# Performance work log

Measured on AMD Instinct MI355X. Metric: run time of the kernel, lower is better.

Reference implementation:

```python
import jax, jax.numpy as jnp
import numpy as np
from jax import lax

B, L, C = 4, 4096, 512
H = 8           # head_num
D = C // H      # head dim = 64
RR = 4          # reduction_ratio -> reducer conv kernel 7, stride 4
KS = 3          # MixFFN depthwise kernel
ER = 4          # expansion ratio -> 2048 channels
EPS = 1e-5      # torch LayerNorm default eps


def _ln(x, g, b):
    # LayerNorm over last axis, affine per-channel
    m = jnp.mean(x, axis=-1, keepdims=True)
    v = jnp.mean(jnp.square(x - m), axis=-1, keepdims=True)
    return (x - m) * lax.rsqrt(v + EPS) * g + b


def setup_inputs() -> dict:
    key = jax.random.key(0)
    ks = jax.random.split(key, 9)
    s = lambda fan: 1.0 / np.sqrt(fan)
    return {
        "x": jax.random.normal(ks[0], (B, L, C), jnp.float32),
        "w_q": jax.random.normal(ks[1], (C, C), jnp.float32) * s(C),
        "w_k": jax.random.normal(ks[2], (C, C), jnp.float32) * s(C),
        "w_v": jax.random.normal(ks[3], (C, C), jnp.float32) * s(C),
        "w_o": jax.random.normal(ks[4], (C, C), jnp.float32) * s(C),
        "w_red": jax.random.normal(ks[5], (C, C, 2 * RR - 1), jnp.float32) * s(C * (2 * RR - 1)),
        "w_ffn1": jax.random.normal(ks[6], (C, C), jnp.float32) * s(C),
        "w_ffn_dw": jax.random.normal(ks[7], (C * ER, 1, KS), jnp.float32) * s(KS),
        "w_ffn2": jax.random.normal(ks[8], (C, C * ER), jnp.float32) * s(C * ER),
        "ln_gamma": jnp.ones((6, C), jnp.float32),
        "ln_beta": jnp.zeros((6, C), jnp.float32),
    }


def reference(x, w_q, w_k, w_v, w_o, w_red, w_ffn1, w_ffn_dw, w_ffn2, ln_gamma, ln_beta):
    # ln indices: 0=ln1(pre-attn), 1=ln(reducer), 2=ln_q, 3=ln_k, 4=ln_v, 5=ln2(pre-ffn)
    residual = x
    h = _ln(x, ln_gamma[0], ln_beta[0])  # B L C

    # --- spatial-reduction for K/V: reflect-pad strided conv + LN ---
    p = (2 * RR - 1) // 2
    hr = jnp.transpose(h, (0, 2, 1))  # B C L
    hr = jnp.pad(hr, ((0, 0), (0, 0), (p, p)), mode="reflect")
    red = lax.conv_general_dilated(hr, w_red, window_strides=(RR,), padding="VALID",
                                   dimension_numbers=("NCH", "OIH", "NCH"))  # B C Lr
    red = jnp.transpose(red, (0, 2, 1))  # B Lr C
    red = _ln(red, ln_gamma[1], ln_beta[1])

    # --- QKV projections + LayerNorms ---
    q = _ln(h @ w_q.T, ln_gamma[2], ln_beta[2])      # B L C
    k = _ln(red @ w_k.T, ln_gamma[3], ln_beta[3])    # B Lr C
    v = _ln(red @ w_v.T, ln_gamma[4], ln_beta[4])    # B Lr C

    Lr = k.shape[1]
    q = q.reshape(B, L, H, D).transpose(0, 2, 1, 3)   # B h L d
    k = k.reshape(B, Lr, H, D).transpose(0, 2, 1, 3)  # B h Lr d
    v = v.reshape(B, Lr, H, D).transpose(0, 2, 1, 3)

    scores = jnp.einsum("bhqd,bhkd->bhqk", q, k) / jnp.sqrt(jnp.float32(D))
    attn = jax.nn.softmax(scores, axis=-1)
    out = jnp.einsum("bhqk,bhkd->bhqd", attn, v)
    out = out.transpose(0, 2, 1, 3).reshape(B, L, C)
    out = out @ w_o.T

    h2 = out + residual
    residual2 = h2
    f = _ln(h2, ln_gamma[5], ln_beta[5])  # B L C

    # --- MixFFN: 1x1 conv -> depthwise reflect conv (groups=C, out=ER*C) -> GELU -> 1x1 conv ---
    f = jnp.transpose(f, (0, 2, 1))  # B C L
    f = jnp.einsum("oi,bil->bol", w_ffn1, f)  # 1x1, C->C
    pk = (KS - 1) // 2
    fp = jnp.pad(f, ((0, 0), (0, 0), (pk, pk)), mode="reflect")
    f = lax.conv_general_dilated(fp, w_ffn_dw, window_strides=(1,), padding="VALID",
                                 dimension_numbers=("NCH", "OIH", "NCH"),
                                 feature_group_count=C)  # B (ER*C) L
    f = jax.nn.gelu(f, approximate=False)  # torch nn.GELU() is exact erf
    f = jnp.einsum("oi,bil->bol", w_ffn2, f)  # 1x1, ER*C->C
    f = jnp.transpose(f, (0, 2, 1))  # B L C

    return f + residual2
```

## Files before the change

### kernel.cpp

```cpp
#include <hip/hip_runtime.h>
#include <math.h>

typedef __attribute__((ext_vector_type(8))) short short8;
typedef __attribute__((ext_vector_type(4))) float f32x4;
typedef unsigned short u16;
typedef unsigned int u32;
typedef unsigned long long u64;

namespace {
constexpr int kB = 4;
constexpr int kL = 4096;
constexpr int kC = 512;
constexpr int kH = 8;
constexpr int kLr = 1024;
constexpr int kCH = 2048;
constexpr int kKred = 3584;
constexpr float kEps = 1e-5f;
}

__device__ __forceinline__ float bf2f(u16 u) { return __uint_as_float(((u32)u) << 16); }
__device__ __forceinline__ u16 f2bf(float f) {
  u32 u = __float_as_uint(f);
  u32 r = (u + 0x7fffu + ((u >> 16) & 1u)) >> 16;
  return (u16)r;
}
__device__ __forceinline__ u32 cvtpk(float lo, float hi) {
  u32 r;
  asm("v_cvt_pk_bf16_f32 %0, %1, %2" : "=v"(r) : "v"(lo), "v"(hi));
  return r;
}

__device__ __forceinline__ void gload_lds16(const void* g, void* l) {
  __builtin_amdgcn_global_load_lds(
      (const __attribute__((address_space(1))) unsigned int*)g,
      (__attribute__((address_space(3))) unsigned int*)l, 16, 0, 0);
}

__device__ __forceinline__ short8 ldsfrag(const u16* base, int row, int col16) {
  return *(const short8*)(base + (size_t)(((row << 3) + (col16 ^ (row & 7))) << 3));
}

__global__ __launch_bounds__(256) void cvt_weights_kernel(
    const float* __restrict__ w_q, const float* __restrict__ w_k,
    const float* __restrict__ w_v, const float* __restrict__ w_o,
    const float* __restrict__ w_f1, const float* __restrict__ w_f2,
    u16* __restrict__ dst) {
  const int i = (blockIdx.x * 256 + threadIdx.x) * 4;
  const int seg = i >> 18;
  const float* src;
  int off;
  if (seg < 5) {
    src = (seg == 0) ? w_q : (seg == 1) ? w_k : (seg == 2) ? w_v : (seg == 3) ? w_o : w_f1;
    off = i & 262143;
  } else {
    src = w_f2;
    off = i - 1310720;
  }
  const float4 v = *(const float4*)(src + off);
  u16 o[4] = {f2bf(v.x), f2bf(v.y), f2bf(v.z), f2bf(v.w)};
  *(u64*)(dst + i) = *(u64*)o;
}

__global__ __launch_bounds__(256) void repack_wred_kernel(const float* __restrict__ src,
                                                          u16* __restrict__ dst) {
  const int idx = blockIdx.x * 256 + threadIdx.x;
  if (idx >= kC * kKred) return;
  const int o = idx / kKred;
  const int rem = idx - o * kKred;
  const int t = rem >> 9;
  const int i = rem & (kC - 1);
  dst[idx] = f2bf(src[(size_t)(o * kC + i) * 7 + t]);
}

__global__ __launch_bounds__(256) void ln_bf16_kernel(const float* __restrict__ in,
                                                      u16* __restrict__ out,
                                                      const float* __restrict__ g,
                                                      const float* __restrict__ be) {
  const int row = blockIdx.x;
  const int tid = threadIdx.x;
  const float2 v = *(const float2*)(in + (size_t)row * kC + tid * 2);
  float s = v.x + v.y;
  float ss = v.x * v.x + v.y * v.y;
#pragma unroll
  for (int off = 32; off > 0; off >>= 1) {
    s += __shfl_down(s, off);
    ss += __shfl_down(ss, off);
  }
  __shared__ float wsum[4][2];
  __shared__ float mi[2];
  const int wave = tid >> 6, lane = tid & 63;
  if (lane == 0) { wsum[wave][0] = s; wsum[wave][1] = ss; }
  __syncthreads();
  if (tid == 0) {
    const float S = wsum[0][0] + wsum[1][0] + wsum[2][0] + wsum[3][0];
    const float SS = wsum[0][1] + wsum[1][1] + wsum[2][1] + wsum[3][1];
    const float mean = S * (1.0f / kC);
    const float var = SS * (1.0f / kC) - mean * mean;
    mi[0] = mean;
    mi[1] = rsqrtf(var + kEps);
  }
  __syncthreads();
  const float mean = mi[0], inv = mi[1];
  const float2 gg = *(const float2*)(g + tid * 2);
  const float2 bb = *(const float2*)(be + tid * 2);
  u16 o2[2] = {f2bf((v.x - mean) * inv * gg.x + bb.x), f2bf((v.y - mean) * inv * gg.y + bb.y)};
  *(u32*)(out + (size_t)row * kC + tid * 2) = *(u32*)o2;
}

__global__ __launch_bounds__(256) void reduce2_ln_kernel(const float* __restrict__ P,
                                                         u16* __restrict__ out,
                                                         const float* __restrict__ g,
                                                         const float* __restrict__ be) {
  const int row = blockIdx.x;
  const int tid = threadIdx.x;
  const size_t stride = (size_t)kB * kLr * kC;
  float2 v = make_float2(0.f, 0.f);
#pragma unroll
  for (int z = 0; z < 2; ++z) {
    const float2 p = *(const float2*)(P + z * stride + (size_t)row * kC + tid * 2);
    v.x += p.x;
    v.y += p.y;
  }
  float s = v.x + v.y;
  float ss = v.x * v.x + v.y * v.y;
#pragma unroll
  for (int off = 32; off > 0; off >>= 1) {
    s += __shfl_down(s, off);
    ss += __shfl_down(ss, off);
  }
  __shared__ float wsum[4][2];
  __shared__ float mi[2];
  const int wave = tid >> 6, lane = tid & 63;
  if (lane == 0) { wsum[wave][0] = s; wsum[wave][1] = ss; }
  __syncthreads();
  if (tid == 0) {
    const float S = wsum[0][0] + wsum[1][0] + wsum[2][0] + wsum[3][0];
    const float SS = wsum[0][1] + wsum[1][1] + wsum[2][1] + wsum[3][1];
    const float mean = S * (1.0f / kC);
    const float var = SS * (1.0f / kC) - mean * mean;
    mi[0] = mean;
    mi[1] = rsqrtf(var + kEps);
  }
  __syncthreads();
  const float mean = mi[0], inv = mi[1];
  const float2 gg = *(const float2*)(g + tid * 2);
  const float2 bb = *(const float2*)(be + tid * 2);
  u16 o2[2] = {f2bf((v.x - mean) * inv * gg.x + bb.x), f2bf((v.y - mean) * inv * gg.y + bb.y)};
  *(u32*)(out + (size_t)row * kC + tid * 2) = *(u32*)o2;
}

__global__ __launch_bounds__(256) void dwgelu_kernel(const u16* __restrict__ f1,
                                                     const float* __restrict__ wdw,
                                                     u16* __restrict__ fdw) {
  const int row = blockIdx.x;
  const int l = row & (kL - 1);
  const int rb = row - l;
  const int cc0 = threadIdx.x * 8;
  const int cg = cc0 >> 2;
  const int lm = (l == 0) ? 1 : l - 1;
  const int lp = (l == kL - 1) ? kL - 2 : l + 1;
  const u32 xm = *(const u32*)(f1 + (size_t)(rb + lm) * kC + cg);
  const u32 x0 = *(const u32*)(f1 + (size_t)(rb + l) * kC + cg);
  const u32 xp = *(const u32*)(f1 + (size_t)(rb + lp) * kC + cg);
  const float xml = bf2f((u16)xm), xmh = bf2f((u16)(xm >> 16));
  const float x0l = bf2f((u16)x0), x0h = bf2f((u16)(x0 >> 16));
  const float xpl = bf2f((u16)xp), xph = bf2f((u16)(xp >> 16));
  float wv[24];
#pragma unroll
  for (int t = 0; t < 6; ++t)
    *(float4*)&wv[t * 4] = *(const float4*)(wdw + (size_t)cc0 * 3 + t * 4);
  short8 pk;
#pragma unroll
  for (int j = 0; j < 8; ++j) {
    const float a_ = (j < 4) ? xml : xmh;
    const float b_ = (j < 4) ? x0l : x0h;
    const float c_ = (j < 4) ? xpl : xph;
    const float dw = wv[j * 3] * a_ + wv[j * 3 + 1] * b_ + wv[j * 3 + 2] * c_;
    pk[j] = (short)f2bf(0.5f * dw * (1.0f + erff(dw * 0.70710678118654752440f)));
  }
  *(short8*)(fdw + (size_t)row * kCH + cc0) = pk;
}

__global__ __launch_bounds__(256) void mgemm_red_kernel(
    const u16* __restrict__ A, const u16* __restrict__ W, float* __restrict__ OutF,
    int M, int N, int K) {
  __shared__ __align__(16) u16 As[128 * 64];
  __shared__ __align__(16) u16 Bs[128 * 64];
  const int tid = threadIdx.x;
  const int lane = tid & 63, w = tid >> 6;
  const int m0 = blockIdx.y * 128, n0 = blockIdx.x * 128;
  const int wm = (w >> 1) * 64, wn = (w & 1) * 64;
  const f32x4 zero = {0.f, 0.f, 0.f, 0.f};
  f32x4 acc[4][4];
#pragma unroll
  for (int i = 0; i < 4; ++i)
#pragma unroll
    for (int j = 0; j < 4; ++j) acc[i][j] = zero;

  const int kc = K / gridDim.z;
  const int kBeg = blockIdx.z * kc, kEnd = kBeg + kc;
  float* outp = OutF + (size_t)blockIdx.z * M * N;

  for (int k0 = kBeg; k0 < kEnd; k0 += 64) {
    __syncthreads();
#pragma unroll
    for (int c = 0; c < 4; ++c) {
      const int ci = w * 4 + c;
      const int idx = ci * 64 + lane;
      const int row = idx >> 3, s = idx & 7;
      const int c16 = s ^ (row & 7);
      gload_lds16(W + (size_t)(n0 + row) * K + k0 + c16 * 8, (char*)Bs + ci * 1024);
    }
#pragma unroll
    for (int c = 0; c < 4; ++c) {
      const int ci = w * 4 + c;
      const int idx = ci * 64 + lane;
      const int row = idx >> 3, s = idx & 7;
      const int c16 = s ^ (row & 7);
      const int m = m0 + row;
      const int b = m >> 10, lr = m & (kLr - 1);
      const int k = k0 + c16 * 8;
      const int t = k >> 9, i = k & (kC - 1);
      int pos = 4 * lr + t - 3;
      pos = pos < 0 ? -pos : (pos >= kL ? 2 * kL - 2 - pos : pos);
      gload_lds16(A + ((size_t)(b << 12) + pos) * kC + i, (char*)As + ci * 1024);
    }
    __syncthreads();
#pragma unroll
    for (int kst = 0; kst < 2; ++kst) {
      short8 af[4], bfr[4];
      const int c16 = kst * 4 + (lane >> 4);
#pragma unroll
      for (int mb = 0; mb < 4; ++mb) af[mb] = ldsfrag(As, wm + mb * 16 + (lane & 15), c16);
#pragma unroll
      for (int nb = 0; nb < 4; ++nb) bfr[nb] = ldsfrag(Bs, wn + nb * 16 + (lane & 15), c16);
#pragma unroll
      for (int mb = 0; mb < 4; ++mb)
#pragma unroll
        for (int nb = 0; nb < 4; ++nb)
          acc[mb][nb] = __builtin_amdgcn_mfma_f32_16x16x32_bf16(af[mb], bfr[nb], acc[mb][nb], 0, 0, 0);
    }
  }
#pragma unroll
  for (int mb = 0; mb < 4; ++mb)
#pragma unroll
    for (int r = 0; r < 4; ++r) {
      const int row = m0 + wm + mb * 16 + ((lane >> 4) << 2) + r;
#pragma unroll
      for (int nb = 0; nb < 4; ++nb)
        outp[(size_t)row * N + n0 + wn + nb * 16 + (lane & 15)] = acc[mb][nb][r];
    }
}

__global__ __launch_bounds__(256) void mgemm_res_kernel(
    const u16* __restrict__ A, const u16* __restrict__ W,
    const float* __restrict__ Res, float* __restrict__ OutF, int M, int N, int K) {
  __shared__ __align__(16) u16 As[128 * 64];
  __shared__ __align__(16) u16 Bs[128 * 64];
  const int tid = threadIdx.x;
  const int lane = tid & 63, w = tid >> 6;
  const int m0 = blockIdx.y * 128, n0 = blockIdx.x * 128;
  const int wm = (w >> 1) * 64, wn = (w & 1) * 64;
  const f32x4 zero = {0.f, 0.f, 0.f, 0.f};
  f32x4 acc[4][4];
#pragma unroll
  for (int i = 0; i < 4; ++i)
#pragma unroll
    for (int j = 0; j < 4; ++j) acc[i][j] = zero;

  for (int k0 = 0; k0 < K; k0 += 64) {
    __syncthreads();
#pragma unroll
    for (int c = 0; c < 4; ++c) {
      const int ci = w * 4 + c;
      const int idx = ci * 64 + lane;
      const int row = idx >> 3, s = idx & 7;
      const int c16 = s ^ (row & 7);
      gload_lds16(W + (size_t)(n0 + row) * K + k0 + c16 * 8, (char*)Bs + ci * 1024);
    }
#pragma unroll
    for (int c = 0; c < 4; ++c) {
      const int ci = w * 4 + c;
      const int idx = ci * 64 + lane;
      const int row = idx >> 3, s = idx & 7;
      const int c16 = s ^ (row & 7);
      gload_lds16(A + (size_t)(m0 + row) * K + k0 + c16 * 8, (char*)As + ci * 1024);
    }
    __syncthreads();
#pragma unroll
    for (int kst = 0; kst < 2; ++kst) {
      short8 af[4], bfr[4];
      const int c16 = kst * 4 + (lane >> 4);
#pragma unroll
      for (int mb = 0; mb < 4; ++mb) af[mb] = ldsfrag(As, wm + mb * 16 + (lane & 15), c16);
#pragma unroll
      for (int nb = 0; nb < 4; ++nb) bfr[nb] = ldsfrag(Bs, wn + nb * 16 + (lane & 15), c16);
#pragma unroll
      for (int mb = 0; mb < 4; ++mb)
#pragma unroll
        for (int nb = 0; nb < 4; ++nb)
          acc[mb][nb] = __builtin_amdgcn_mfma_f32_16x16x32_bf16(af[mb], bfr[nb], acc[mb][nb], 0, 0, 0);
    }
  }
#pragma unroll
  for (int mb = 0; mb < 4; ++mb)
#pragma unroll
    for (int r = 0; r < 4; ++r) {
      const int row = m0 + wm + mb * 16 + ((lane >> 4) << 2) + r;
#pragma unroll
      for (int nb = 0; nb < 4; ++nb) {
        const size_t off = (size_t)row * N + n0 + wn + nb * 16 + (lane & 15);
        OutF[off] = acc[mb][nb][r] + Res[off];
      }
    }
}

template <int EPI>
__global__ __launch_bounds__(512) void gemm512_kernel(
    const u16* __restrict__ A, const u16* __restrict__ W,
    const float* __restrict__ Res, float* __restrict__ OutF,
    u16* __restrict__ OutB, u16* __restrict__ OutB2,
    int K, const float* __restrict__ gam, const float* __restrict__ bet, float oscale) {
  constexpr bool RES_ = (EPI == 3);
  constexpr bool LN_ = (EPI == 1 || EPI == 2 || EPI == 3);
  __shared__ __align__(16) u16 As[64 * 64];
  __shared__ __align__(16) u16 Bs[512 * 64];
  const int tid = threadIdx.x;
  const int lane = tid & 63, w = tid >> 6;
  const int l15 = lane & 15, g = lane >> 4;
  const int m0 = blockIdx.y * 64;
  const int n0 = blockIdx.x * 512;
  const int wn = w << 6;
  const f32x4 zero = {0.f, 0.f, 0.f, 0.f};
  f32x4 acc[4][4];
#pragma unroll
  for (int i = 0; i < 4; ++i)
#pragma unroll
    for (int j = 0; j < 4; ++j) acc[i][j] = zero;

  for (int k0 = 0; k0 < K; k0 += 64) {
    __syncthreads();
#pragma unroll
    for (int c = 0; c < 8; ++c) {
      const int cg = (w << 3) + c;
      const int idx = (cg << 6) + lane;
      const int row = idx >> 3, sl = idx & 7;
      const int c16 = sl ^ (row & 7);
      gload_lds16(W + (size_t)(n0 + row) * K + k0 + (c16 << 3), (char*)Bs + cg * 1024);
    }
    {
      const int idx = (w << 6) + lane;
      const int row = idx >> 3, sl = idx & 7;
      const int c16 = sl ^ (row & 7);
      gload_lds16(A + (size_t)(m0 + row) * K + k0 + (c16 << 3), (char*)As + w * 1024);
    }
    __syncthreads();
#pragma unroll
    for (int kst = 0; kst < 2; ++kst) {
      const int c16 = (kst << 2) + g;
      short8 af[4], bfr[4];
#pragma unroll
      for (int mb = 0; mb < 4; ++mb) af[mb] = ldsfrag(As, (mb << 4) + l15, c16);
#pragma unroll
      for (int nb = 0; nb < 4; ++nb) bfr[nb] = ldsfrag(Bs, wn + (nb << 4) + l15, c16);
#pragma unroll
      for (int mb = 0; mb < 4; ++mb)
#pragma unroll
        for (int nb = 0; nb < 4; ++nb)
          acc[mb][nb] = __builtin_amdgcn_mfma_f32_16x16x32_bf16(af[mb], bfr[nb], acc[mb][nb], 0, 0, 0);
    }
  }

  if (RES_) {
#pragma unroll
    for (int mb = 0; mb < 4; ++mb)
#pragma unroll
      for (int r = 0; r < 4; ++r) {
        const int grow = m0 + (mb << 4) + (g << 2) + r;
#pragma unroll
        for (int nb = 0; nb < 4; ++nb)
          acc[mb][nb][r] += Res[(size_t)grow * kC + wn + (nb << 4) + l15];
      }
  }
  float* rs = (float*)As;
  float* rs2 = rs + 512;
  float2* minv = (float2*)(rs2 + 512);
  if (LN_) {
    __syncthreads();
#pragma unroll
    for (int mb = 0; mb < 4; ++mb)
#pragma unroll
      for (int r = 0; r < 4; ++r) {
        float s = acc[mb][0][r] + acc[mb][1][r] + acc[mb][2][r] + acc[mb][3][r];
        float s2 = acc[mb][0][r] * acc[mb][0][r] + acc[mb][1][r] * acc[mb][1][r] +
                   acc[mb][2][r] * acc[mb][2][r] + acc[mb][3][r] * acc[mb][3][r];
        s += __shfl_xor(s, 1); s += __shfl_xor(s, 2); s += __shfl_xor(s, 4); s += __shfl_xor(s, 8);
        s2 += __shfl_xor(s2, 1); s2 += __shfl_xor(s2, 2); s2 += __shfl_xor(s2, 4); s2 += __shfl_xor(s2, 8);
        if (l15 == 0) {
          const int row = (mb << 4) + (g << 2) + r;
          rs[(w << 6) + row] = s;
          rs2[(w << 6) + row] = s2;
        }
      }
    __syncthreads();
    if (tid < 64) {
      float S = 0.f, SS = 0.f;
#pragma unroll
      for (int w8 = 0; w8 < 8; ++w8) { S += rs[(w8 << 6) + tid]; SS += rs2[(w8 << 6) + tid]; }
      const float mean = S * (1.0f / 512.0f);
      const float var = SS * (1.0f / 512.0f) - mean * mean;
      minv[tid] = make_float2(mean, rsqrtf(var + kEps));
    }
    __syncthreads();
  }
  float g4[4], b4[4];
  if (LN_) {
    const float* gp = (EPI == 2 && blockIdx.x) ? gam + kC : gam;
    const float* bp = (EPI == 2 && blockIdx.x) ? bet + kC : bet;
#pragma unroll
    for (int nb = 0; nb < 4; ++nb) {
      const int cc = wn + (nb << 4) + l15;
      g4[nb] = gp[cc];
      b4[nb] = bp[cc];
    }
  }
#pragma unroll
  for (int mb = 0; mb < 4; ++mb) {
#pragma unroll
    for (int r = 0; r < 4; ++r) {
      const int row = (mb << 4) + (g << 2) + r;
      const int grow = m0 + row;
      float2 mi = make_float2(0.f, 0.f);
      if (LN_) mi = minv[row];
#pragma unroll
      for (int nb = 0; nb < 4; ++nb) {
        const int cc = wn + (nb << 4) + l15;
        const float vv = acc[mb][nb][r];
        if (EPI == 0) {
          OutB[(size_t)grow * kC + cc] = f2bf(vv);
        } else if (EPI == 1) {
          OutB[(size_t)grow * kC + cc] = f2bf(((vv - mi.x) * mi.y * g4[nb] + b4[nb]) * oscale);
        } else if (EPI == 2) {
          const float lv = (vv - mi.x) * mi.y * g4[nb] + b4[nb];
          if (blockIdx.x == 0) {
            OutB[(size_t)grow * kC + cc] = f2bf(lv);
          } else {
            const int b = grow >> 10, lr = grow & (kLr - 1);
            const int hh = cc >> 6, d = cc & 63;
            OutB2[((size_t)((b << 3) + hh) * 64 + d) * kLr + lr] = f2bf(lv);
          }
        } else {
          OutF[(size_t)grow * kC + cc] = vv;
          OutB[(size_t)grow * kC + cc] = f2bf((vv - mi.x) * mi.y * g4[nb] + b4[nb]);
        }
      }
    }
  }
}

__global__ __launch_bounds__(256) void attn_mfma_kernel(
    const u16* __restrict__ q, const u16* __restrict__ k,
    const u16* __restrict__ vt, u16* __restrict__ o) {
  __shared__ __align__(16) u16 Qs[128 * 64];
  __shared__ __align__(16) u16 Ks[2][64 * 64];
  __shared__ __align__(16) u16 Vs[2][64 * 64];
  __shared__ __align__(16) u16 Ps[4][32 * 64];
  const int tid = threadIdx.x;
  const int lane = tid & 63, w = tid >> 6;
  const int qt = blockIdx.x, h = blockIdx.y, b = blockIdx.z;
  const int q0 = qt << 7;
  const int l15 = lane & 15, g = lane >> 4;

#pragma unroll
  for (int c = 0; c < 4; ++c) {
    const int ci = (w << 2) + c;
    const int a16 = (ci << 6) + lane;
    const int r = a16 >> 3, sl = a16 & 7;
    gload_lds16(q + (size_t)((b << 12) + q0 + r) * kC + (h << 6) + ((sl ^ (r & 7)) << 3),
                (char*)Qs + ci * 1024);
  }
#pragma unroll
  for (int c = 0; c < 2; ++c) {
    const int ci = (w << 1) + c;
    const int a16 = (ci << 6) + lane;
    const int r = a16 >> 3, sl = a16 & 7;
    const int c16 = sl ^ (r & 7);
    gload_lds16(k + (size_t)((b << 10) + r) * kC + (h << 6) + (c16 << 3), (char*)Ks[0] + ci * 1024);
    gload_lds16(vt + (size_t)(((b << 3) + h) * 64 + r) * kLr + (c16 << 3), (char*)Vs[0] + ci * 1024);
  }

  const f32x4 zero = {0.f, 0.f, 0.f, 0.f};
  float m2[2] = {-1e30f, -1e30f};
  float l2[2] = {0.f, 0.f};
  f32x4 accO[2][4];
#pragma unroll
  for (int s_ = 0; s_ < 2; ++s_)
#pragma unroll
    for (int d = 0; d < 4; ++d) accO[s_][d] = zero;

  __syncthreads();

  for (int t = 0; t < kLr / 64; ++t) {
    const int cur = t & 1;
    if (t < kLr / 64 - 1) {
      const int kv0 = (t + 1) << 6;
#pragma unroll
      for (int c = 0; c < 2; ++c) {
        const int ci = (w << 1) + c;
        const int a16 = (ci << 6) + lane;
        const int r = a16 >> 3, sl = a16 & 7;
        const int c16 = sl ^ (r & 7);
        gload_lds16(k + (size_t)((b << 10) + kv0 + r) * kC + (h << 6) + (c16 << 3),
                    (char*)Ks[cur ^ 1] + ci * 1024);
        gload_lds16(vt + (size_t)(((b << 3) + h) * 64 + r) * kLr + kv0 + (c16 << 3),
                    (char*)Vs[cur ^ 1] + ci * 1024);
      }
    }
    f32x4 st[2][4];
#pragma unroll
    for (int s_ = 0; s_ < 2; ++s_)
#pragma unroll
      for (int nb = 0; nb < 4; ++nb) st[s_][nb] = zero;
    __builtin_amdgcn_s_setprio(1);
#pragma unroll
    for (int kst = 0; kst < 2; ++kst) {
      const int c16 = (kst << 2) + g;
      const short8 bq0 = ldsfrag(Qs, (w << 5) + l15, c16);
      const short8 bq1 = ldsfrag(Qs, (w << 5) + 16 + l15, c16);
#pragma unroll
      for (int nb = 0; nb < 4; ++nb) {
        const short8 ak = ldsfrag(Ks[cur], (nb << 4) + l15, c16);
        st[0][nb] = __builtin_amdgcn_mfma_f32_16x16x32_bf16(ak, bq0, st[0][nb], 0, 0, 0);
        st[1][nb] = __builtin_amdgcn_mfma_f32_16x16x32_bf16(ak, bq1, st[1][nb], 0, 0, 0);
      }
    }
    __builtin_amdgcn_s_setprio(0);
    bool sk[2];
#pragma unroll
    for (int s_ = 0; s_ < 2; ++s_) {
      float pm = -1e30f;
#pragma unroll
      for (int nb = 0; nb < 4; ++nb)
#pragma unroll
        for (int r = 0; r < 4; ++r) pm = fmaxf(pm, st[s_][nb][r]);
      pm = fmaxf(pm, __shfl_xor(pm, 16));
      pm = fmaxf(pm, __shfl_xor(pm, 32));
      sk[s_] = __all(pm - m2[s_] <= 8.0f);
      float scl = 1.0f;
      if (!sk[s_]) {
        const float mnew = fmaxf(m2[s_], pm);
        scl = __expf(m2[s_] - mnew);
        m2[s_] = mnew;
      }
      float ps = 0.f;
#pragma unroll
      for (int nb = 0; nb < 4; ++nb)
#pragma unroll
        for (int r = 0; r < 4; ++r) {
          const float e = __expf(st[s_][nb][r] - m2[s_]);
          st[s_][nb][r] = e;
          ps += e;
        }
      ps += __shfl_xor(ps, 16);
      ps += __shfl_xor(ps, 32);
      l2[s_] = l2[s_] * scl + ps;
      char* pw = (char*)&Ps[w][0];
      const int row = (s_ << 4) + l15;
#pragma unroll
      for (int nb = 0; nb < 4; ++nb) {
        const u32 lo = cvtpk(st[s_][nb][0], st[s_][nb][1]);
        const u32 hi = cvtpk(st[s_][nb][2], st[s_][nb][3]);
        const int slot = ((nb << 1) + (g >> 1)) ^ (row & 7);
        *(u64*)(pw + (row << 7) + (slot << 4) + ((g & 1) << 3)) = ((u64)hi << 32) | lo;
      }
      if (!sk[s_]) {
        const float scl2 = scl;
        float scA[4];
#pragma unroll
        for (int r = 0; r < 4; ++r) scA[r] = __shfl(scl2, (g << 2) + r);
#pragma unroll
        for (int d = 0; d < 4; ++d)
#pragma unroll
          for (int r = 0; r < 4; ++r) accO[s_][d][r] *= scA[r];
      }
    }
    __builtin_amdgcn_s_setprio(1);
#pragma unroll
    for (int kvs = 0; kvs < 2; ++kvs) {
      const int c16 = (kvs << 2) + g;
      const short8 ap0 = ldsfrag(&Ps[w][0], l15, c16);
      const short8 ap1 = ldsfrag(&Ps[w][0], 16 + l15, c16);
#pragma unroll
      for (int d = 0; d < 4; ++d) {
        const short8 bv = ldsfrag(Vs[cur], (d << 4) + l15, c16);
        accO[0][d] = __builtin_amdgcn_mfma_f32_16x16x32_bf16(ap0, bv, accO[0][d], 0, 0, 0);
        accO[1][d] = __builtin_amdgcn_mfma_f32_16x16x32_bf16(ap1, bv, accO[1][d], 0, 0, 0);
      }
    }
    __builtin_amdgcn_s_setprio(0);
    __syncthreads();
  }
#pragma unroll
  for (int s_ = 0; s_ < 2; ++s_) {
    float li[4];
#pragma unroll
    for (int r = 0; r < 4; ++r) li[r] = 1.0f / __shfl(l2[s_], (g << 2) + r);
    const int qg = (b << 12) + q0 + (w << 5) + (s_ << 4) + (g << 2);
#pragma unroll
    for (int d = 0; d < 4; ++d)
#pragma unroll
      for (int r = 0; r < 4; ++r)
        o[(size_t)(qg + r) * kC + (h << 6) + (d << 4) + l15] = f2bf(accO[s_][d][r] * li[r]);
  }
}

extern "C" void kernel_launch(void* const* d_in, const int* in_sizes, int n_in,
                              void* d_out, int out_size, void* d_ws, size_t ws_size,
                              hipStream_t stream) {
  const float* x      = (const float*)d_in[0];
  const float* w_q    = (const float*)d_in[1];
  const float* w_k    = (const float*)d_in[2];
  const float* w_v    = (const float*)d_in[3];
  const float* w_o    = (const float*)d_in[4];
  const float* w_red  = (const float*)d_in[5];
  const float* w_ffn1 = (const float*)d_in[6];
  const float* w_dw   = (const float*)d_in[7];
  const float* w_ffn2 = (const float*)d_in[8];
  const float* gam    = (const float*)d_in[9];
  const float* bet    = (const float*)d_in[10];
  float* out = (float*)d_out;

  const size_t nBLC = (size_t)kB * kL * kC;
  const size_t nBLrC = (size_t)kB * kLr * kC;
  u16* us = (u16*)d_ws;
  u16* wqb   = us;
  u16* wkb   = wqb + 262144;
  u16* wob   = wkb + 2 * 262144;
  u16* wf1b  = wob + 262144;
  u16* wf2b  = wf1b + 262144;
  u16* wredb = wf2b + 1048576;
  u16* h_b   = wredb + 1835008;
  u16* q_b   = h_b + nBLC;
  u16* red_b = q_b + nBLC;
  u16* k_b   = red_b + nBLrC;
  u16* vt_b  = k_b + nBLrC;
  float* S   = (float*)(vt_b + nBLrC);
  u16* fdw   = q_b;

  cvt_weights_kernel<<<2304, 256, 0, stream>>>(w_q, w_k, w_v, w_o, w_ffn1, w_ffn2, wqb);
  repack_wred_kernel<<<7168, 256, 0, stream>>>(w_red, wredb);

  ln_bf16_kernel<<<kB * kL, 256, 0, stream>>>(x, h_b, gam, bet);
  mgemm_red_kernel<<<dim3(4, 32, 2), 256, 0, stream>>>(h_b, wredb, S, kB * kLr, kC, kKred);
  reduce2_ln_kernel<<<kB * kLr, 256, 0, stream>>>(S, red_b, gam + kC, bet + kC);
  gemm512_kernel<1><<<dim3(1, 256), 512, 0, stream>>>(
      h_b, wqb, nullptr, nullptr, q_b, nullptr, kC, gam + 2 * kC, bet + 2 * kC, 0.125f);
  gemm512_kernel<2><<<dim3(2, 64), 512, 0, stream>>>(
      red_b, wkb, nullptr, nullptr, k_b, vt_b, kC, gam + 3 * kC, bet + 3 * kC, 1.0f);
  attn_mfma_kernel<<<dim3(kL / 128, kH, kB), 256, 0, stream>>>(q_b, k_b, vt_b, h_b);
  gemm512_kernel<3><<<dim3(1, 256), 512, 0, stream>>>(
      h_b, wob, x, out, q_b, nullptr, kC, gam + 5 * kC, bet + 5 * kC, 1.0f);
  gemm512_kernel<0><<<dim3(1, 256), 512, 0, stream>>>(
      q_b, wf1b, nullptr, nullptr, h_b, nullptr, kC, nullptr, nullptr, 1.0f);
  dwgelu_kernel<<<kB * kL, 256, 0, stream>>>(h_b, w_dw, fdw);
  mgemm_res_kernel<<<dim3(4, 128), 256, 0, stream>>>(fdw, wf2b, out, out, kB * kL, kC, kCH);
}
```

Before: 320.2 us.

## Double-buffer GEMM LDS tiles and halve attention query tile per block

All three GEMM kernels now keep two LDS buffers and issue the loads for the next K-tile before computing on the current one, so global-to-LDS transfers overlap MFMA work and each iteration needs one barrier instead of two. The attention kernel drops from 128 to 64 queries per block (16 per wave), which doubles the grid and lowers register and LDS use per block. The cost is double the GEMM LDS footprint (about 72KB for gemm512), which can lower occupancy, and more reloads of K/V across the extra attention blocks.

```diff
diff --git a/kernel.cpp b/kernel.cpp
--- a/kernel.cpp
+++ b/kernel.cpp
@@ -184,8 +184,8 @@
 __global__ __launch_bounds__(256) void mgemm_red_kernel(
     const u16* __restrict__ A, const u16* __restrict__ W, float* __restrict__ OutF,
     int M, int N, int K) {
-  __shared__ __align__(16) u16 As[128 * 64];
-  __shared__ __align__(16) u16 Bs[128 * 64];
+  __shared__ __align__(16) u16 As[2][128 * 64];
+  __shared__ __align__(16) u16 Bs[2][128 * 64];
   const int tid = threadIdx.x;
   const int lane = tid & 63, w = tid >> 6;
   const int m0 = blockIdx.y * 128, n0 = blockIdx.x * 128;
@@ -198,48 +198,48 @@
     for (int j = 0; j < 4; ++j) acc[i][j] = zero;
 
   const int kc = K / gridDim.z;
-  const int kBeg = blockIdx.z * kc, kEnd = kBeg + kc;
+  const int kBeg = blockIdx.z * kc;
   float* outp = OutF + (size_t)blockIdx.z * M * N;
 
-  for (int k0 = kBeg; k0 < kEnd; k0 += 64) {
-    __syncthreads();
+  auto stage = [&](int buf, int k0) {
 #pragma unroll
     for (int c = 0; c < 4; ++c) {
       const int ci = w * 4 + c;
       const int idx = ci * 64 + lane;
       const int row = idx >> 3, s = idx & 7;
       const int c16 = s ^ (row & 7);
-      gload_lds16(W + (size_t)(n0 + row) * K + k0 + c16 * 8, (char*)Bs + ci * 1024);
-    }
-#pragma unroll
-    for (int c = 0; c < 4; ++c) {
-      const int ci = w * 4 + c;
-      const int idx = ci * 64 + lane;
-      const int row = idx >> 3, s = idx & 7;
-      const int c16 = s ^ (row & 7);
+      gload_lds16(W + (size_t)(n0 + row) * K + k0 + c16 * 8, (char*)Bs[buf] + ci * 1024);
       const int m = m0 + row;
       const int b = m >> 10, lr = m & (kLr - 1);
       const int k = k0 + c16 * 8;
       const int t = k >> 9, i = k & (kC - 1);
       int pos = 4 * lr + t - 3;
       pos = pos < 0 ? -pos : (pos >= kL ? 2 * kL - 2 - pos : pos);
-      gload_lds16(A + ((size_t)(b << 12) + pos) * kC + i, (char*)As + ci * 1024);
-    }
-    __syncthreads();
+      gload_lds16(A + ((size_t)(b << 12) + pos) * kC + i, (char*)As[buf] + ci * 1024);
+    }
+  };
+
+  const int nk = kc >> 6;
+  stage(0, kBeg);
+  __syncthreads();
+  for (int t = 0; t < nk; ++t) {
+    const int cur = t & 1;
+    if (t + 1 < nk) stage(cur ^ 1, kBeg + ((t + 1) << 6));
 #pragma unroll
     for (int kst = 0; kst < 2; ++kst) {
       short8 af[4], bfr[4];
       const int c16 = kst * 4 + (lane >> 4);
 #pragma unroll
-      for (int mb = 0; mb < 4; ++mb) af[mb] = ldsfrag(As, wm + mb * 16 + (lane & 15), c16);
-#pragma unroll
-      for (int nb = 0; nb < 4; ++nb) bfr[nb] = ldsfrag(Bs, wn + nb * 16 + (lane & 15), c16);
+      for (int mb = 0; mb < 4; ++mb) af[mb] = ldsfrag(As[cur], wm + mb * 16 + (lane & 15), c16);
+#pragma unroll
+      for (int nb = 0; nb < 4; ++nb) bfr[nb] = ldsfrag(Bs[cur], wn + nb * 16 + (lane & 15), c16);
 #pragma unroll
       for (int mb = 0; mb < 4; ++mb)
 #pragma unroll
         for (int nb = 0; nb < 4; ++nb)
           acc[mb][nb] = __builtin_amdgcn_mfma_f32_16x16x32_bf16(af[mb], bfr[nb], acc[mb][nb], 0, 0, 0);
     }
+    __syncthreads();
   }
 #pragma unroll
   for (int mb = 0; mb < 4; ++mb)
@@ -255,8 +255,8 @@
 __global__ __launch_bounds__(256) void mgemm_res_kernel(
     const u16* __restrict__ A, const u16* __restrict__ W,
     const float* __restrict__ Res, float* __restrict__ OutF, int M, int N, int K) {
-  __shared__ __align__(16) u16 As[128 * 64];
-  __shared__ __align__(16) u16 Bs[128 * 64];
+  __shared__ __align__(16) u16 As[2][128 * 64];
+  __shared__ __align__(16) u16 Bs[2][128 * 64];
   const int tid = threadIdx.x;
   const int lane = tid & 63, w = tid >> 6;
   const int m0 = blockIdx.y * 128, n0 = blockIdx.x * 128;
@@ -268,39 +268,39 @@
 #pragma unroll
     for (int j = 0; j < 4; ++j) acc[i][j] = zero;
 
-  for (int k0 = 0; k0 < K; k0 += 64) {
-    __syncthreads();
+  auto stage = [&](int buf, int k0) {
 #pragma unroll
     for (int c = 0; c < 4; ++c) {
       const int ci = w * 4 + c;
       const int idx = ci * 64 + lane;
       const int row = idx >> 3, s = idx & 7;
       const int c16 = s ^ (row & 7);
-      gload_lds16(W + (size_t)(n0 + row) * K + k0 + c16 * 8, (char*)Bs + ci * 1024);
-    }
-#pragma unroll
-    for (int c = 0; c < 4; ++c) {
-      const int ci = w * 4 + c;
-      const int idx = ci * 64 + lane;
-      const int row = idx >> 3, s = idx & 7;
-      const int c16 = s ^ (row & 7);
-      gload_lds16(A + (size_t)(m0 + row) * K + k0 + c16 * 8, (char*)As + ci * 1024);
-    }
-    __syncthreads();
+      gload_lds16(W + (size_t)(n0 + row) * K + k0 + c16 * 8, (char*)Bs[buf] + ci * 1024);
+      gload_lds16(A + (size_t)(m0 + row) * K + k0 + c16 * 8, (char*)As[buf] + ci * 1024);
+    }
+  };
+
+  const int nk = K >> 6;
+  stage(0, 0);
+  __syncthreads();
+  for (int t = 0; t < nk; ++t) {
+    const int cur = t & 1;
+    if (t + 1 < nk) stage(cur ^ 1, (t + 1) << 6);
 #pragma unroll
     for (int kst = 0; kst < 2; ++kst) {
       short8 af[4], bfr[4];
       const int c16 = kst * 4 + (lane >> 4);
 #pragma unroll
-      for (int mb = 0; mb < 4; ++mb) af[mb] = ldsfrag(As, wm + mb * 16 + (lane & 15), c16);
-#pragma unroll
-      for (int nb = 0; nb < 4; ++nb) bfr[nb] = ldsfrag(Bs, wn + nb * 16 + (lane & 15), c16);
+      for (int mb = 0; mb < 4; ++mb) af[mb] = ldsfrag(As[cur], wm + mb * 16 + (lane & 15), c16);
+#pragma unroll
+      for (int nb = 0; nb < 4; ++nb) bfr[nb] = ldsfrag(Bs[cur], wn + nb * 16 + (lane & 15), c16);
 #pragma unroll
       for (int mb = 0; mb < 4; ++mb)
 #pragma unroll
         for (int nb = 0; nb < 4; ++nb)
           acc[mb][nb] = __builtin_amdgcn_mfma_f32_16x16x32_bf16(af[mb], bfr[nb], acc[mb][nb], 0, 0, 0);
     }
+    __syncthreads();
   }
 #pragma unroll
   for (int mb = 0; mb < 4; ++mb)
@@ -323,8 +323,8 @@
     int K, const float* __restrict__ gam, const float* __restrict__ bet, float oscale) {
   constexpr bool RES_ = (EPI == 3);
   constexpr bool LN_ = (EPI == 1 || EPI == 2 || EPI == 3);
-  __shared__ __align__(16) u16 As[64 * 64];
-  __shared__ __align__(16) u16 Bs[512 * 64];
+  __shared__ __align__(16) u16 As[2][64 * 64];
+  __shared__ __align__(16) u16 Bs[2][512 * 64];
   const int tid = threadIdx.x;
   const int lane = tid & 63, w = tid >> 6;
   const int l15 = lane & 15, g = lane >> 4;
@@ -338,37 +338,42 @@
 #pragma unroll
     for (int j = 0; j < 4; ++j) acc[i][j] = zero;
 
-  for (int k0 = 0; k0 < K; k0 += 64) {
-    __syncthreads();
+  auto stage = [&](int buf, int k0) {
 #pragma unroll
     for (int c = 0; c < 8; ++c) {
       const int cg = (w << 3) + c;
       const int idx = (cg << 6) + lane;
       const int row = idx >> 3, sl = idx & 7;
       const int c16 = sl ^ (row & 7);
-      gload_lds16(W + (size_t)(n0 + row) * K + k0 + (c16 << 3), (char*)Bs + cg * 1024);
-    }
-    {
-      const int idx = (w << 6) + lane;
-      const int row = idx >> 3, sl = idx & 7;
-      const int c16 = sl ^ (row & 7);
-      gload_lds16(A + (size_t)(m0 + row) * K + k0 + (c16 << 3), (char*)As + w * 1024);
-    }
-    __syncthreads();
+      gload_lds16(W + (size_t)(n0 + row) * K + k0 + (c16 << 3), (char*)Bs[buf] + cg * 1024);
+    }
+    const int idx = (w << 6) + lane;
+    const int row = idx >> 3, sl = idx & 7;
+    const int c16 = sl ^ (row & 7);
+    gload_lds16(A + (size_t)(m0 + row) * K + k0 + (c16 << 3), (char*)As[buf] + w * 1024);
+  };
+
+  const int nk = K >> 6;
+  stage(0, 0);
+  __syncthreads();
+  for (int t = 0; t < nk; ++t) {
+    const int cur = t & 1;
+    if (t + 1 < nk) stage(cur ^ 1, (t + 1) << 6);
 #pragma unroll
     for (int kst = 0; kst < 2; ++kst) {
       const int c16 = (kst << 2) + g;
       short8 af[4], bfr[4];
 #pragma unroll
-      for (int mb = 0; mb < 4; ++mb) af[mb] = ldsfrag(As, (mb << 4) + l15, c16);
-#pragma unroll
-      for (int nb = 0; nb < 4; ++nb) bfr[nb] = ldsfrag(Bs, wn + (nb << 4) + l15, c16);
+      for (int mb = 0; mb < 4; ++mb) af[mb] = ldsfrag(As[cur], (mb << 4) + l15, c16);
+#pragma unroll
+      for (int nb = 0; nb < 4; ++nb) bfr[nb] = ldsfrag(Bs[cur], wn + (nb << 4) + l15, c16);
 #pragma unroll
       for (int mb = 0; mb < 4; ++mb)
 #pragma unroll
         for (int nb = 0; nb < 4; ++nb)
           acc[mb][nb] = __builtin_amdgcn_mfma_f32_16x16x32_bf16(af[mb], bfr[nb], acc[mb][nb], 0, 0, 0);
     }
+    __syncthreads();
   }
 
   if (RES_) {
@@ -382,11 +387,10 @@
           acc[mb][nb][r] += Res[(size_t)grow * kC + wn + (nb << 4) + l15];
       }
   }
-  float* rs = (float*)As;
+  float* rs = (float*)As[0];
   float* rs2 = rs + 512;
   float2* minv = (float2*)(rs2 + 512);
   if (LN_) {
-    __syncthreads();
 #pragma unroll
     for (int mb = 0; mb < 4; ++mb)
 #pragma unroll
@@ -461,19 +465,19 @@
 __global__ __launch_bounds__(256) void attn_mfma_kernel(
     const u16* __restrict__ q, const u16* __restrict__ k,
     const u16* __restrict__ vt, u16* __restrict__ o) {
-  __shared__ __align__(16) u16 Qs[128 * 64];
+  __shared__ __align__(16) u16 Qs[64 * 64];
   __shared__ __align__(16) u16 Ks[2][64 * 64];
   __shared__ __align__(16) u16 Vs[2][64 * 64];
-  __shared__ __align__(16) u16 Ps[4][32 * 64];
+  __shared__ __align__(16) u16 Ps[4][16 * 64];
   const int tid = threadIdx.x;
   const int lane = tid & 63, w = tid >> 6;
   const int qt = blockIdx.x, h = blockIdx.y, b = blockIdx.z;
-  const int q0 = qt << 7;
+  const int q0 = qt << 6;
   const int l15 = lane & 15, g = lane >> 4;
 
 #pragma unroll
-  for (int c = 0; c < 4; ++c) {
-    const int ci = (w << 2) + c;
+  for (int c = 0; c < 2; ++c) {
+    const int ci = (w << 1) + c;
     const int a16 = (ci << 6) + lane;
     const int r = a16 >> 3, sl = a16 & 7;
     gload_lds16(q + (size_t)((b << 12) + q0 + r) * kC + (h << 6) + ((sl ^ (r & 7)) << 3),
@@ -490,13 +494,8 @@
   }
 
   const f32x4 zero = {0.f, 0.f, 0.f, 0.f};
-  float m2[2] = {-1e30f, -1e30f};
-  float l2[2] = {0.f, 0.f};
-  f32x4 accO[2][4];
-#pragma unroll
-  for (int s_ = 0; s_ < 2; ++s_)
-#pragma unroll
-    for (int d = 0; d < 4; ++d) accO[s_][d] = zero;
+  float m1 = -1e30f, l1 = 0.f;
+  f32x4 accO[4] = {zero, zero, zero, zero};
 
   __syncthreads();
 
@@ -516,102 +515,87 @@
                     (char*)Vs[cur ^ 1] + ci * 1024);
       }
     }
-    f32x4 st[2][4];
-#pragma unroll
-    for (int s_ = 0; s_ < 2; ++s_)
-#pragma unroll
-      for (int nb = 0; nb < 4; ++nb) st[s_][nb] = zero;
+    f32x4 st[4] = {zero, zero, zero, zero};
     __builtin_amdgcn_s_setprio(1);
 #pragma unroll
     for (int kst = 0; kst < 2; ++kst) {
       const int c16 = (kst << 2) + g;
-      const short8 bq0 = ldsfrag(Qs, (w << 5) + l15, c16);
-      const short8 bq1 = ldsfrag(Qs, (w << 5) + 16 + l15, c16);
+      const short8 bq = ldsfrag(Qs, (w << 4) + l15, c16);
 #pragma unroll
       for (int nb = 0; nb < 4; ++nb) {
         const short8 ak = ldsfrag(Ks[cur], (nb << 4) + l15, c16);
-        st[0][nb] = __builtin_amdgcn_mfma_f32_16x16x32_bf16(ak, bq0, st[0][nb], 0, 0, 0);
-        st[1][nb] = __builtin_amdgcn_mfma_f32_16x16x32_bf16(ak, bq1, st[1][nb], 0, 0, 0);
+        st[nb] = __builtin_amdgcn_mfma_f32_16x16x32_bf16(ak, bq, st[nb], 0, 0, 0);
       }
     }
     __builtin_amdgcn_s_setprio(0);
-    bool sk[2];
-#pragma unroll
-    for (int s_ = 0; s_ < 2; ++s_) {
+    {
       float pm = -1e30f;
 #pragma unroll
       for (int nb = 0; nb < 4; ++nb)
 #pragma unroll
-        for (int r = 0; r < 4; ++r) pm = fmaxf(pm, st[s_][nb][r]);
+        for (int r = 0; r < 4; ++r) pm = fmaxf(pm, st[nb][r]);
       pm = fmaxf(pm, __shfl_xor(pm, 16));
       pm = fmaxf(pm, __shfl_xor(pm, 32));
-      sk[s_] = __all(pm - m2[s_] <= 8.0f);
+      const bool sk = __all(pm - m1 <= 8.0f);
       float scl = 1.0f;
-      if (!sk[s_]) {
-        const float mnew = fmaxf(m2[s_], pm);
-        scl = __expf(m2[s_] - mnew);
-        m2[s_] = mnew;
+      if (!sk) {
+        const float mnew = fmaxf(m1, pm);
+        scl = __expf(m1 - mnew);
+        m1 = mnew;
       }
       float ps = 0.f;
 #pragma unroll
       for (int nb = 0; nb < 4; ++nb)
 #pragma unroll
         for (int r = 0; r < 4; ++r) {
-          const float e = __expf(st[s_][nb][r] - m2[s_]);
-          st[s_][nb][r] = e;
+          const float e = __expf(st[nb][r] - m1);
+          st[nb][r] = e;
           ps += e;
         }
       ps += __shfl_xor(ps, 16);
       ps += __shfl_xor(ps, 32);
-      l2[s_] = l2[s_] * scl + ps;
+      l1 = l1 * scl + ps;
       char* pw = (char*)&Ps[w][0];
-      const int row = (s_ << 4) + l15;
 #pragma unroll
       for (int nb = 0; nb < 4; ++nb) {
-        const u32 lo = cvtpk(st[s_][nb][0], st[s_][nb][1]);
-        const u32 hi = cvtpk(st[s_][nb][2], st[s_][nb][3]);
-        const int slot = ((nb << 1) + (g >> 1)) ^ (row & 7);
-        *(u64*)(pw + (row << 7) + (slot << 4) + ((g & 1) << 3)) = ((u64)hi << 32) | lo;
-      }
-      if (!sk[s_]) {
-        const float scl2 = scl;
+        const u32 lo = cvtpk(st[nb][0], st[nb][1]);
+        const u32 hi = cvtpk(st[nb][2], st[nb][3]);
+        const int slot = ((nb << 1) + (g >> 1)) ^ (l15 & 7);
+        *(u64*)(pw + (l15 << 7) + (slot << 4) + ((g & 1) << 3)) = ((u64)hi << 32) | lo;
+      }
+      if (!sk) {
         float scA[4];
 #pragma unroll
-        for (int r = 0; r < 4; ++r) scA[r] = __shfl(scl2, (g << 2) + r);
+        for (int r = 0; r < 4; ++r) scA[r] = __shfl(scl, (g << 2) + r);
 #pragma unroll
         for (int d = 0; d < 4; ++d)
 #pragma unroll
-          for (int r = 0; r < 4; ++r) accO[s_][d][r] *= scA[r];
+          for (int r = 0; r < 4; ++r) accO[d][r] *= scA[r];
       }
     }
     __builtin_amdgcn_s_setprio(1);
 #pragma unroll
     for (int kvs = 0; kvs < 2; ++kvs) {
       const int c16 = (kvs << 2) + g;
-      const short8 ap0 = ldsfrag(&Ps[w][0], l15, c16);
-      const short8 ap1 = ldsfrag(&Ps[w][0], 16 + l15, c16);
+      const short8 ap = ldsfrag(&Ps[w][0], l15, c16);
 #pragma unroll
       for (int d = 0; d < 4; ++d) {
         const short8 bv = ldsfrag(Vs[cur], (d << 4) + l15, c16);
-        accO[0][d] = __builtin_amdgcn_mfma_f32_16x16x32_bf16(ap0, bv, accO[0][d], 0, 0, 0);
-        accO[1][d] = __builtin_amdgcn_mfma_f32_16x16x32_bf16(ap1, bv, accO[1][d], 0, 0, 0);
+        accO[d] = __builtin_amdgcn_mfma_f32_16x16x32_bf16(ap, bv, accO[d], 0, 0, 0);
       }
     }
     __builtin_amdgcn_s_setprio(0);
     __syncthreads();
   }
-#pragma unroll
-  for (int s_ = 0; s_ < 2; ++s_) {
-    float li[4];
-#pragma unroll
-    for (int r = 0; r < 4; ++r) li[r] = 1.0f / __shfl(l2[s_], (g << 2) + r);
-    const int qg = (b << 12) + q0 + (w << 5) + (s_ << 4) + (g << 2);
-#pragma unroll
-    for (int d = 0; d < 4; ++d)
-#pragma unroll
-      for (int r = 0; r < 4; ++r)
-        o[(size_t)(qg + r) * kC + (h << 6) + (d << 4) + l15] = f2bf(accO[s_][d][r] * li[r]);
-  }
+  float li[4];
+#pragma unroll
+  for (int r = 0; r < 4; ++r) li[r] = 1.0f / __shfl(l1, (g << 2) + r);
+  const int qg = (b << 12) + q0 + (w << 4) + (g << 2);
+#pragma unroll
+  for (int d = 0; d < 4; ++d)
+#pragma unroll
+    for (int r = 0; r < 4; ++r)
+      o[(size_t)(qg + r) * kC + (h << 6) + (d << 4) + l15] = f2bf(accO[d][r] * li[r]);
 }
 
 extern "C" void kernel_launch(void* const* d_in, const int* in_sizes, int n_in,
@@ -657,7 +641,7 @@
       h_b, wqb, nullptr, nullptr, q_b, nullptr, kC, gam + 2 * kC, bet + 2 * kC, 0.125f);
   gemm512_kernel<2><<<dim3(2, 64), 512, 0, stream>>>(
       red_b, wkb, nullptr, nullptr, k_b, vt_b, kC, gam + 3 * kC, bet + 3 * kC, 1.0f);
-  attn_mfma_kernel<<<dim3(kL / 128, kH, kB), 256, 0, stream>>>(q_b, k_b, vt_b, h_b);
+  attn_mfma_kernel<<<dim3(kL / 64, kH, kB), 256, 0, stream>>>(q_b, k_b, vt_b, h_b);
   gemm512_kernel<3><<<dim3(1, 256), 512, 0, stream>>>(
       h_b, wob, x, out, q_b, nullptr, kC, gam + 5 * kC, bet + 5 * kC, 1.0f);
   gemm512_kernel<0><<<dim3(1, 256), 512, 0, stream>>>(
```

Result: faster. 308.4 us (-3.7%).
